# Kernel tuning notes

Measured on AMD Instinct MI355X. Metric: run time of the kernel, lower is better.

## Reference

```python
import jax, jax.numpy as jnp
import numpy as np

N_EMBD = 1024
D_FF = 4096
N_EXPERTS = 8
TOP_K = 2


def setup_inputs() -> dict:
    key = jax.random.key(0)
    k1, k2, k3, k4 = jax.random.split(key, 4)
    x = jax.random.normal(k1, (1, 2048, N_EMBD), dtype=jnp.float32)
    mask = jnp.ones((2048, N_EXPERTS), dtype=jnp.float32)
    Wr = jax.random.normal(k2, (N_EMBD, N_EXPERTS), dtype=jnp.float32) * 0.02
    W1 = jax.random.normal(k3, (N_EXPERTS, N_EMBD, D_FF), dtype=jnp.float32) * 0.02
    W2 = jax.random.normal(k4, (N_EXPERTS, D_FF, N_EMBD), dtype=jnp.float32) * 0.02
    return {"x": x, "mask": mask, "Wr": Wr, "W1": W1, "W2": W2}


def reference(x, mask, Wr, W1, W2):
    T = x.shape[0] * x.shape[1]
    xs = x.reshape(T, N_EMBD)                      # [T, d]
    router_logits = (xs @ Wr) * mask               # [T, E], masked as in MaskedMoE
    all_probs = jax.nn.softmax(router_logits, axis=-1)  # softmax_topk order
    weights, selected = jax.lax.top_k(all_probs, TOP_K)  # [T, K]
    # combine[t, e] = sum of routing weights where token t selected expert e
    combine = jnp.zeros((T, N_EXPERTS), dtype=xs.dtype)
    combine = combine.at[jnp.arange(T)[:, None], selected].add(weights)
    results = jnp.zeros_like(xs)
    for e in range(N_EXPERTS):  # fixed small expert count
        h = jax.nn.gelu(xs @ W1[e])                # [T, d_ff]
        out = h @ W2[e]                            # [T, d]
        results = results + combine[:, e:e + 1] * out
    return results.reshape(x.shape)
```

## Files before the change

kernel.cpp:

```cpp
#include <hip/hip_runtime.h>
#include <hip/hip_bf16.h>


#define T_TOK 2048
#define D_EMB 1024
#define DFF   4096
#define NE    8

typedef _Float16 f16x8 __attribute__((ext_vector_type(8)));
typedef _Float16 f16x4 __attribute__((ext_vector_type(4)));
typedef float    f32x4 __attribute__((ext_vector_type(4)));

__device__ __forceinline__ float gelu_tanh(float x) {
    const float c = 0.7978845608028654f;
    float x3 = x * x * x;
    return 0.5f * x * (1.0f + tanhf(c * (x + 0.044715f * x3)));
}

__device__ __forceinline__ void gll(const void* g, void* l) {
    __builtin_amdgcn_global_load_lds((__attribute__((address_space(1))) void*)g,
                                     (__attribute__((address_space(3))) void*)l,
                                     16, 0, 0);
}

__global__ void k_zero(int* counts) {
    if (threadIdx.x < NE) counts[threadIdx.x] = 0;
}

__global__ __launch_bounds__(256) void k_cvt_x(const float4* __restrict__ x4,
                                               _Float16* __restrict__ xh) {
    int i = blockIdx.x * 256 + threadIdx.x;
    float4 v = x4[i];
    f16x4 o;
    o[0] = (_Float16)v.x; o[1] = (_Float16)v.y;
    o[2] = (_Float16)v.z; o[3] = (_Float16)v.w;
    *(f16x4*)(xh + (size_t)i * 4) = o;
}

__global__ __launch_bounds__(256) void k_transpose(
    const float* __restrict__ src, _Float16* __restrict__ dst,
    int src_ld, int dst_ld, int src_k0, int src_n0) {
    __shared__ float tile[64][65];
    int e = blockIdx.z;
    const float* S = src + (size_t)e * 4194304;
    _Float16* D = dst + (size_t)e * 2097152;
    int t = threadIdx.x;
    int kb = src_k0 + blockIdx.y * 64;
    int nb = src_n0 + blockIdx.x * 64;
#pragma unroll
    for (int i = 0; i < 4; i++) {
        int r = (t >> 4) + i * 16;
        int c = (t & 15) * 4;
        float4 v = *(const float4*)(S + (size_t)(kb + r) * src_ld + nb + c);
        tile[r][c + 0] = v.x; tile[r][c + 1] = v.y;
        tile[r][c + 2] = v.z; tile[r][c + 3] = v.w;
    }
    __syncthreads();
    int drb = blockIdx.x * 64, dcb = blockIdx.y * 64;
#pragma unroll
    for (int j = 0; j < 2; j++) {
        int idx = j * 256 + t;
        int n = idx >> 3, kc = idx & 7;
        f16x8 o;
#pragma unroll
        for (int u = 0; u < 8; u++) o[u] = (_Float16)tile[kc * 8 + u][n];
        *(f16x8*)(D + (size_t)(drb + n) * dst_ld + dcb + kc * 8) = o;
    }
}

__global__ __launch_bounds__(256) void k_router(
    const float* __restrict__ x, const float* __restrict__ mask,
    const float* __restrict__ Wr,
    int* __restrict__ counts, int* __restrict__ elist, float* __restrict__ wlist) {
    int wave = threadIdx.x >> 6;
    int lane = threadIdx.x & 63;
    int t = blockIdx.x * 4 + wave;
    if (t >= T_TOK) return;

    float acc[NE];
#pragma unroll
    for (int e = 0; e < NE; e++) acc[e] = 0.f;
    const float* xr = x + (size_t)t * D_EMB;
    for (int c = 0; c < D_EMB / 64; c++) {
        int i = c * 64 + lane;
        float xv = xr[i];
        const float* wr = Wr + (size_t)i * NE;
#pragma unroll
        for (int e = 0; e < NE; e++) acc[e] += xv * wr[e];
    }
#pragma unroll
    for (int e = 0; e < NE; e++) {
#pragma unroll
        for (int off = 32; off > 0; off >>= 1)
            acc[e] += __shfl_xor(acc[e], off);
    }
    if (lane == 0) {
        float p[NE];
        float mx = -1e30f;
#pragma unroll
        for (int e = 0; e < NE; e++) {
            p[e] = acc[e] * mask[t * NE + e];
            mx = fmaxf(mx, p[e]);
        }
        float s = 0.f;
#pragma unroll
        for (int e = 0; e < NE; e++) { p[e] = expf(p[e] - mx); s += p[e]; }
#pragma unroll
        for (int e = 0; e < NE; e++) p[e] /= s;
        int e0 = 0; float b0 = p[0];
#pragma unroll
        for (int e = 1; e < NE; e++) if (p[e] > b0) { b0 = p[e]; e0 = e; }
        int e1 = -1; float b1 = -1.f;
#pragma unroll
        for (int e = 0; e < NE; e++) if (e != e0 && p[e] > b1) { b1 = p[e]; e1 = e; }

        int pos0 = atomicAdd(&counts[e0], 1);
        elist[e0 * T_TOK + pos0] = t;
        wlist[e0 * T_TOK + pos0] = b0;
        int pos1 = atomicAdd(&counts[e1], 1);
        elist[e1 * T_TOK + pos1] = t;
        wlist[e1 * T_TOK + pos1] = b1;
    }
}

__global__ void k_prefix(const int* __restrict__ counts, int* __restrict__ base) {
    if (threadIdx.x == 0) {
        int s = 0;
        for (int e = 0; e < NE; e++) { base[e] = s; s += counts[e]; }
        base[NE] = s;
    }
}

__global__ __launch_bounds__(256) void k_gemm1(
    const _Float16* __restrict__ xh, const _Float16* __restrict__ BT,
    const int* __restrict__ counts, const int* __restrict__ base,
    const int* __restrict__ elist, _Float16* __restrict__ H, int n0g) {
    int e = blockIdx.z;
    int cnt = counts[e];
    int p0 = blockIdx.y * 128;
    if (p0 >= cnt) return;
    int n0 = blockIdx.x * 128;
    const _Float16* B = BT + (size_t)e * 2097152;

    __shared__ _Float16 As[128 * 32];
    __shared__ _Float16 Bs[128 * 32];
    __shared__ int ttok[128];

    int tid = threadIdx.x;
    if (tid < 128) ttok[tid] = elist[e * T_TOK + min(p0 + tid, cnt - 1)];
    __syncthreads();

    int w = tid >> 6, lane = tid & 63;
    int c0 = tid, c1 = tid + 256;
    const _Float16* pA0 = xh + (size_t)ttok[c0 >> 2] * D_EMB + (c0 & 3) * 8;
    const _Float16* pA1 = xh + (size_t)ttok[c1 >> 2] * D_EMB + (c1 & 3) * 8;
    const _Float16* pB0 = B + (size_t)(n0 + (c0 >> 2)) * 1024 + (c0 & 3) * 8;
    const _Float16* pB1 = B + (size_t)(n0 + (c1 >> 2)) * 1024 + (c1 & 3) * 8;
    _Float16* ldsA0 = As + (w * 64) * 8;
    _Float16* ldsA1 = As + (256 + w * 64) * 8;
    _Float16* ldsB0 = Bs + (w * 64) * 8;
    _Float16* ldsB1 = Bs + (256 + w * 64) * 8;

    int wm = w >> 1, wn = w & 1;
    int lhi = lane >> 4, llo = lane & 15;
    const _Float16* arp = As + ((wm * 64 + llo) * 32 + lhi * 8);
    const _Float16* brp = Bs + ((wn * 64 + llo) * 32 + lhi * 8);

    f32x4 acc[4][4] = {};
    for (int k0 = 0; k0 < D_EMB; k0 += 32) {
        __syncthreads();
        gll(pA0, ldsA0); gll(pA1, ldsA1);
        gll(pB0, ldsB0); gll(pB1, ldsB1);
        pA0 += 32; pA1 += 32; pB0 += 32; pB1 += 32;
        __syncthreads();
        f16x8 a[4], b[4];
#pragma unroll
        for (int i = 0; i < 4; i++) {
            a[i] = *(const f16x8*)(arp + i * 512);
            b[i] = *(const f16x8*)(brp + i * 512);
        }
#pragma unroll
        for (int mt = 0; mt < 4; mt++)
#pragma unroll
            for (int nt = 0; nt < 4; nt++)
                acc[mt][nt] = __builtin_amdgcn_mfma_f32_16x16x32_f16(a[mt], b[nt], acc[mt][nt], 0, 0, 0);
    }

    int rowbase = base[e];
#pragma unroll
    for (int mt = 0; mt < 4; mt++) {
#pragma unroll
        for (int i = 0; i < 4; i++) {
            int p = p0 + wm * 64 + mt * 16 + lhi * 4 + i;
            if (p < cnt) {
                size_t rowoff = (size_t)(rowbase + p) * DFF + n0g + n0 + wn * 64 + llo;
#pragma unroll
                for (int nt = 0; nt < 4; nt++)
                    H[rowoff + nt * 16] = (_Float16)gelu_tanh(acc[mt][nt][i]);
            }
        }
    }
}

__global__ __launch_bounds__(256) void k_gemm2(
    const _Float16* __restrict__ H, const _Float16* __restrict__ BT,
    const int* __restrict__ counts, const int* __restrict__ base,
    const int* __restrict__ elist, const float* __restrict__ wlist,
    float* __restrict__ out, int kh) {
    int e = blockIdx.z;
    int cnt = counts[e];
    int p0 = blockIdx.y * 128;
    if (p0 >= cnt) return;
    int n0 = blockIdx.x * 128;
    const _Float16* B = BT + (size_t)e * 2097152;
    int rowbase = base[e];

    __shared__ _Float16 As[128 * 32];
    __shared__ _Float16 Bs[128 * 32];
    __shared__ int ttok[128];
    __shared__ float twt[128];

    int tid = threadIdx.x;
    if (tid < 128) {
        int p = min(p0 + tid, cnt - 1);
        ttok[tid] = elist[e * T_TOK + p];
        twt[tid]  = wlist[e * T_TOK + p];
    }

    int w = tid >> 6, lane = tid & 63;
    int c0 = tid, c1 = tid + 256;
    int r0 = rowbase + min(p0 + (c0 >> 2), cnt - 1);
    int r1 = rowbase + min(p0 + (c1 >> 2), cnt - 1);
    const _Float16* pA0 = H + (size_t)r0 * DFF + kh + (c0 & 3) * 8;
    const _Float16* pA1 = H + (size_t)r1 * DFF + kh + (c1 & 3) * 8;
    const _Float16* pB0 = B + (size_t)(n0 + (c0 >> 2)) * 2048 + (c0 & 3) * 8;
    const _Float16* pB1 = B + (size_t)(n0 + (c1 >> 2)) * 2048 + (c1 & 3) * 8;
    _Float16* ldsA0 = As + (w * 64) * 8;
    _Float16* ldsA1 = As + (256 + w * 64) * 8;
    _Float16* ldsB0 = Bs + (w * 64) * 8;
    _Float16* ldsB1 = Bs + (256 + w * 64) * 8;

    int wm = w >> 1, wn = w & 1;
    int lhi = lane >> 4, llo = lane & 15;
    const _Float16* arp = As + ((wm * 64 + llo) * 32 + lhi * 8);
    const _Float16* brp = Bs + ((wn * 64 + llo) * 32 + lhi * 8);

    f32x4 acc[4][4] = {};
    for (int k0 = 0; k0 < 2048; k0 += 32) {
        __syncthreads();
        gll(pA0, ldsA0); gll(pA1, ldsA1);
        gll(pB0, ldsB0); gll(pB1, ldsB1);
        pA0 += 32; pA1 += 32; pB0 += 32; pB1 += 32;
        __syncthreads();
        f16x8 a[4], b[4];
#pragma unroll
        for (int i = 0; i < 4; i++) {
            a[i] = *(const f16x8*)(arp + i * 512);
            b[i] = *(const f16x8*)(brp + i * 512);
        }
#pragma unroll
        for (int mt = 0; mt < 4; mt++)
#pragma unroll
            for (int nt = 0; nt < 4; nt++)
                acc[mt][nt] = __builtin_amdgcn_mfma_f32_16x16x32_f16(a[mt], b[nt], acc[mt][nt], 0, 0, 0);
    }

#pragma unroll
    for (int mt = 0; mt < 4; mt++) {
#pragma unroll
        for (int i = 0; i < 4; i++) {
            int pl = wm * 64 + mt * 16 + lhi * 4 + i;
            int p = p0 + pl;
            if (p < cnt) {
                int t = ttok[pl];
                float wgt = twt[pl];
                size_t o = (size_t)t * D_EMB + n0 + wn * 64 + llo;
#pragma unroll
                for (int nt = 0; nt < 4; nt++)
                    atomicAdd(&out[o + nt * 16], acc[mt][nt][i] * wgt);
            }
        }
    }
}

extern "C" void kernel_launch(void* const* d_in, const int* in_sizes, int n_in,
                              void* d_out, int out_size, void* d_ws, size_t ws_size,
                              hipStream_t stream) {
    const float* x    = (const float*)d_in[0];
    const float* mask = (const float*)d_in[1];
    const float* Wr   = (const float*)d_in[2];
    const float* W1   = (const float*)d_in[3];
    const float* W2   = (const float*)d_in[4];
    float* out = (float*)d_out;

    char* ws = (char*)d_ws;
    int*      counts = (int*)(ws + 0);
    int*      base   = (int*)(ws + 256);
    int*      elist  = (int*)(ws + 512);
    float*    wlist  = (float*)(ws + 512 + 65536);
    _Float16* xh     = (_Float16*)(ws + 262144);
    _Float16* H      = (_Float16*)(ws + 262144 + 4194304);
    _Float16* Wbuf   = (_Float16*)(ws + 262144 + 4194304 + 33554432);

    hipMemsetAsync(d_out, 0, (size_t)T_TOK * D_EMB * 4, stream);
    k_zero<<<1, 64, 0, stream>>>(counts);
    k_cvt_x<<<T_TOK * D_EMB / 4 / 256, 256, 0, stream>>>((const float4*)x, xh);
    k_router<<<T_TOK / 4, 256, 0, stream>>>(x, mask, Wr, counts, elist, wlist);
    k_prefix<<<1, 64, 0, stream>>>(counts, base);

    for (int h = 0; h < 2; h++) {
        k_transpose<<<dim3(32, 16, NE), 256, 0, stream>>>(W1, Wbuf, DFF, 1024, 0, h * 2048);
        k_gemm1<<<dim3(16, 16, NE), 256, 0, stream>>>(xh, Wbuf, counts, base, elist, H, h * 2048);
    }
    for (int h = 0; h < 2; h++) {
        k_transpose<<<dim3(16, 32, NE), 256, 0, stream>>>(W2, Wbuf, D_EMB, 2048, h * 2048, 0);
        k_gemm2<<<dim3(8, 16, NE), 256, 0, stream>>>(H, Wbuf, counts, base, elist, wlist, out, h * 2048);
    }
}
```

Baseline: 568.2 us.

## Replace atomic scatter with per-row outputs and final weighted combine; full-size weight buffers

GEMM2 now writes per-expert-row partial outputs for each K-half into two fp32 buffers, and a new final kernel gathers each token's two expert rows, sums the halves and applies the routing weights. This removes the fp32 atomicAdd scatter and the output memset. W1 and W2 are each transposed once into their own full-size buffers, so GEMM1 runs as a single launch over the whole FFN width. GELU now uses an exp-based tanh. The cost is extra workspace and an additional pass that reads about 32MB of intermediates.

```diff
diff --git a/kernel.cpp b/kernel.cpp
--- a/kernel.cpp
+++ b/kernel.cpp
@@ -13,8 +13,10 @@
 
 __device__ __forceinline__ float gelu_tanh(float x) {
     const float c = 0.7978845608028654f;
-    float x3 = x * x * x;
-    return 0.5f * x * (1.0f + tanhf(c * (x + 0.044715f * x3)));
+    float z = c * (x + 0.044715f * x * x * x);
+    float u = __expf(2.0f * z);
+    float th = (u - 1.0f) / (u + 1.0f);
+    return 0.5f * x * (1.0f + th);
 }
 
 __device__ __forceinline__ void gll(const void* g, void* l) {
@@ -39,14 +41,14 @@
 
 __global__ __launch_bounds__(256) void k_transpose(
     const float* __restrict__ src, _Float16* __restrict__ dst,
-    int src_ld, int dst_ld, int src_k0, int src_n0) {
+    int src_ld, int dst_ld) {
     __shared__ float tile[64][65];
     int e = blockIdx.z;
     const float* S = src + (size_t)e * 4194304;
-    _Float16* D = dst + (size_t)e * 2097152;
+    _Float16* D = dst + (size_t)e * 4194304;
     int t = threadIdx.x;
-    int kb = src_k0 + blockIdx.y * 64;
-    int nb = src_n0 + blockIdx.x * 64;
+    int kb = blockIdx.y * 64;
+    int nb = blockIdx.x * 64;
 #pragma unroll
     for (int i = 0; i < 4; i++) {
         int r = (t >> 4) + i * 16;
@@ -56,7 +58,6 @@
         tile[r][c + 2] = v.z; tile[r][c + 3] = v.w;
     }
     __syncthreads();
-    int drb = blockIdx.x * 64, dcb = blockIdx.y * 64;
 #pragma unroll
     for (int j = 0; j < 2; j++) {
         int idx = j * 256 + t;
@@ -64,14 +65,15 @@
         f16x8 o;
 #pragma unroll
         for (int u = 0; u < 8; u++) o[u] = (_Float16)tile[kc * 8 + u][n];
-        *(f16x8*)(D + (size_t)(drb + n) * dst_ld + dcb + kc * 8) = o;
+        *(f16x8*)(D + (size_t)(nb + n) * dst_ld + kb + kc * 8) = o;
     }
 }
 
 __global__ __launch_bounds__(256) void k_router(
     const float* __restrict__ x, const float* __restrict__ mask,
     const float* __restrict__ Wr,
-    int* __restrict__ counts, int* __restrict__ elist, float* __restrict__ wlist) {
+    int* __restrict__ counts, int* __restrict__ elist,
+    int* __restrict__ tok_e, int* __restrict__ tok_p, float* __restrict__ tok_w) {
     int wave = threadIdx.x >> 6;
     int lane = threadIdx.x & 63;
     int t = blockIdx.x * 4 + wave;
@@ -116,10 +118,10 @@
 
         int pos0 = atomicAdd(&counts[e0], 1);
         elist[e0 * T_TOK + pos0] = t;
-        wlist[e0 * T_TOK + pos0] = b0;
+        tok_e[t * 2 + 0] = e0; tok_p[t * 2 + 0] = pos0; tok_w[t * 2 + 0] = b0;
         int pos1 = atomicAdd(&counts[e1], 1);
         elist[e1 * T_TOK + pos1] = t;
-        wlist[e1 * T_TOK + pos1] = b1;
+        tok_e[t * 2 + 1] = e1; tok_p[t * 2 + 1] = pos1; tok_w[t * 2 + 1] = b1;
     }
 }
 
@@ -134,13 +136,13 @@
 __global__ __launch_bounds__(256) void k_gemm1(
     const _Float16* __restrict__ xh, const _Float16* __restrict__ BT,
     const int* __restrict__ counts, const int* __restrict__ base,
-    const int* __restrict__ elist, _Float16* __restrict__ H, int n0g) {
+    const int* __restrict__ elist, _Float16* __restrict__ H) {
     int e = blockIdx.z;
     int cnt = counts[e];
     int p0 = blockIdx.y * 128;
     if (p0 >= cnt) return;
     int n0 = blockIdx.x * 128;
-    const _Float16* B = BT + (size_t)e * 2097152;
+    const _Float16* B = BT + (size_t)e * 4194304;
 
     __shared__ _Float16 As[128 * 32];
     __shared__ _Float16 Bs[128 * 32];
@@ -193,7 +195,7 @@
         for (int i = 0; i < 4; i++) {
             int p = p0 + wm * 64 + mt * 16 + lhi * 4 + i;
             if (p < cnt) {
-                size_t rowoff = (size_t)(rowbase + p) * DFF + n0g + n0 + wn * 64 + llo;
+                size_t rowoff = (size_t)(rowbase + p) * DFF + n0 + wn * 64 + llo;
 #pragma unroll
                 for (int nt = 0; nt < 4; nt++)
                     H[rowoff + nt * 16] = (_Float16)gelu_tanh(acc[mt][nt][i]);
@@ -205,36 +207,27 @@
 __global__ __launch_bounds__(256) void k_gemm2(
     const _Float16* __restrict__ H, const _Float16* __restrict__ BT,
     const int* __restrict__ counts, const int* __restrict__ base,
-    const int* __restrict__ elist, const float* __restrict__ wlist,
-    float* __restrict__ out, int kh) {
+    float* __restrict__ O, int kh) {
     int e = blockIdx.z;
     int cnt = counts[e];
     int p0 = blockIdx.y * 128;
     if (p0 >= cnt) return;
     int n0 = blockIdx.x * 128;
-    const _Float16* B = BT + (size_t)e * 2097152;
+    const _Float16* B = BT + (size_t)e * 4194304;
     int rowbase = base[e];
 
     __shared__ _Float16 As[128 * 32];
     __shared__ _Float16 Bs[128 * 32];
-    __shared__ int ttok[128];
-    __shared__ float twt[128];
 
     int tid = threadIdx.x;
-    if (tid < 128) {
-        int p = min(p0 + tid, cnt - 1);
-        ttok[tid] = elist[e * T_TOK + p];
-        twt[tid]  = wlist[e * T_TOK + p];
-    }
-
     int w = tid >> 6, lane = tid & 63;
     int c0 = tid, c1 = tid + 256;
     int r0 = rowbase + min(p0 + (c0 >> 2), cnt - 1);
     int r1 = rowbase + min(p0 + (c1 >> 2), cnt - 1);
     const _Float16* pA0 = H + (size_t)r0 * DFF + kh + (c0 & 3) * 8;
     const _Float16* pA1 = H + (size_t)r1 * DFF + kh + (c1 & 3) * 8;
-    const _Float16* pB0 = B + (size_t)(n0 + (c0 >> 2)) * 2048 + (c0 & 3) * 8;
-    const _Float16* pB1 = B + (size_t)(n0 + (c1 >> 2)) * 2048 + (c1 & 3) * 8;
+    const _Float16* pB0 = B + (size_t)(n0 + (c0 >> 2)) * 4096 + kh + (c0 & 3) * 8;
+    const _Float16* pB1 = B + (size_t)(n0 + (c1 >> 2)) * 4096 + kh + (c1 & 3) * 8;
     _Float16* ldsA0 = As + (w * 64) * 8;
     _Float16* ldsA1 = As + (256 + w * 64) * 8;
     _Float16* ldsB0 = Bs + (w * 64) * 8;
@@ -269,18 +262,37 @@
     for (int mt = 0; mt < 4; mt++) {
 #pragma unroll
         for (int i = 0; i < 4; i++) {
-            int pl = wm * 64 + mt * 16 + lhi * 4 + i;
-            int p = p0 + pl;
+            int p = p0 + wm * 64 + mt * 16 + lhi * 4 + i;
             if (p < cnt) {
-                int t = ttok[pl];
-                float wgt = twt[pl];
-                size_t o = (size_t)t * D_EMB + n0 + wn * 64 + llo;
+                size_t o = (size_t)(rowbase + p) * D_EMB + n0 + wn * 64 + llo;
 #pragma unroll
                 for (int nt = 0; nt < 4; nt++)
-                    atomicAdd(&out[o + nt * 16], acc[mt][nt][i] * wgt);
+                    O[o + nt * 16] = acc[mt][nt][i];
             }
         }
     }
+}
+
+__global__ __launch_bounds__(256) void k_final(
+    const float* __restrict__ O0, const float* __restrict__ O1,
+    const int* __restrict__ base,
+    const int* __restrict__ tok_e, const int* __restrict__ tok_p,
+    const float* __restrict__ tok_w, float* __restrict__ out) {
+    int t = blockIdx.x;
+    int r0 = base[tok_e[t * 2 + 0]] + tok_p[t * 2 + 0];
+    int r1 = base[tok_e[t * 2 + 1]] + tok_p[t * 2 + 1];
+    float w0 = tok_w[t * 2 + 0], w1 = tok_w[t * 2 + 1];
+    int i = threadIdx.x * 4;
+    float4 a0 = *(const float4*)(O0 + (size_t)r0 * D_EMB + i);
+    float4 b0 = *(const float4*)(O1 + (size_t)r0 * D_EMB + i);
+    float4 a1 = *(const float4*)(O0 + (size_t)r1 * D_EMB + i);
+    float4 b1 = *(const float4*)(O1 + (size_t)r1 * D_EMB + i);
+    float4 o;
+    o.x = w0 * (a0.x + b0.x) + w1 * (a1.x + b1.x);
+    o.y = w0 * (a0.y + b0.y) + w1 * (a1.y + b1.y);
+    o.z = w0 * (a0.z + b0.z) + w1 * (a1.z + b1.z);
+    o.w = w0 * (a0.w + b0.w) + w1 * (a1.w + b1.w);
+    *(float4*)(out + (size_t)t * D_EMB + i) = o;
 }
 
 extern "C" void kernel_launch(void* const* d_in, const int* in_sizes, int n_in,
@@ -294,26 +306,29 @@
     float* out = (float*)d_out;
 
     char* ws = (char*)d_ws;
+    const size_t MB = 1024 * 1024;
     int*      counts = (int*)(ws + 0);
     int*      base   = (int*)(ws + 256);
-    int*      elist  = (int*)(ws + 512);
-    float*    wlist  = (float*)(ws + 512 + 65536);
-    _Float16* xh     = (_Float16*)(ws + 262144);
-    _Float16* H      = (_Float16*)(ws + 262144 + 4194304);
-    _Float16* Wbuf   = (_Float16*)(ws + 262144 + 4194304 + 33554432);
-
-    hipMemsetAsync(d_out, 0, (size_t)T_TOK * D_EMB * 4, stream);
+    int*      elist  = (int*)(ws + 1024);
+    int*      tok_e  = (int*)(ws + 1024 + 65536);
+    int*      tok_p  = (int*)(ws + 1024 + 65536 + 16384);
+    float*    tok_w  = (float*)(ws + 1024 + 65536 + 32768);
+    _Float16* xh     = (_Float16*)(ws + 1 * MB);
+    _Float16* W1T    = (_Float16*)(ws + 8 * MB);
+    _Float16* W2T    = (_Float16*)(ws + 72 * MB);
+    _Float16* H      = (_Float16*)(ws + 136 * MB);
+    float*    O0     = (float*)(ws + 168 * MB);
+    float*    O1     = (float*)(ws + 184 * MB);
+
     k_zero<<<1, 64, 0, stream>>>(counts);
+    k_router<<<T_TOK / 4, 256, 0, stream>>>(x, mask, Wr, counts, elist, tok_e, tok_p, tok_w);
+    k_prefix<<<1, 64, 0, stream>>>(counts, base);
     k_cvt_x<<<T_TOK * D_EMB / 4 / 256, 256, 0, stream>>>((const float4*)x, xh);
-    k_router<<<T_TOK / 4, 256, 0, stream>>>(x, mask, Wr, counts, elist, wlist);
-    k_prefix<<<1, 64, 0, stream>>>(counts, base);
-
-    for (int h = 0; h < 2; h++) {
-        k_transpose<<<dim3(32, 16, NE), 256, 0, stream>>>(W1, Wbuf, DFF, 1024, 0, h * 2048);
-        k_gemm1<<<dim3(16, 16, NE), 256, 0, stream>>>(xh, Wbuf, counts, base, elist, H, h * 2048);
-    }
-    for (int h = 0; h < 2; h++) {
-        k_transpose<<<dim3(16, 32, NE), 256, 0, stream>>>(W2, Wbuf, D_EMB, 2048, h * 2048, 0);
-        k_gemm2<<<dim3(8, 16, NE), 256, 0, stream>>>(H, Wbuf, counts, base, elist, wlist, out, h * 2048);
-    }
-}
+    k_transpose<<<dim3(64, 16, NE), 256, 0, stream>>>(W1, W1T, DFF, 1024);
+    k_transpose<<<dim3(16, 64, NE), 256, 0, stream>>>(W2, W2T, D_EMB, 4096);
+
+    k_gemm1<<<dim3(32, 16, NE), 256, 0, stream>>>(xh, W1T, counts, base, elist, H);
+    k_gemm2<<<dim3(8, 16, NE), 256, 0, stream>>>(H, W2T, counts, base, O0, 0);
+    k_gemm2<<<dim3(8, 16, NE), 256, 0, stream>>>(H, W2T, counts, base, O1, 2048);
+    k_final<<<T_TOK, 256, 0, stream>>>(O0, O1, base, tok_e, tok_p, tok_w, out);
+}
```

Result: faster. 543.3 us (-4.4%).
